# Optimization experiments

Measured on AMD Instinct MI355X. Metric: run time of the kernel, lower is better.

Reference implementation:

```python
import jax, jax.numpy as jnp
import numpy as np

EPS = 1e-8

def setup_inputs() -> dict:
    key = jax.random.key(0)
    ks = jax.random.split(key, 10)
    N, IN, Z, C, H = 8192, 512, 128, 64, 50
    x = jax.random.normal(ks[0], (N, IN), dtype=jnp.float32)
    c = jax.random.randint(ks[1], (N, 1), 0, C, dtype=jnp.int64)
    z = jax.random.normal(ks[2], (N, Z), dtype=jnp.float32)
    # f_x MLP params (Linear(IN,50) -> ReLU -> Linear(50,Z))
    W1 = jax.random.normal(ks[3], (IN, H), dtype=jnp.float32) / np.sqrt(IN)
    b1 = jax.random.normal(ks[4], (H,), dtype=jnp.float32) * 0.01
    W2 = jax.random.normal(ks[5], (H, Z), dtype=jnp.float32) / np.sqrt(H)
    b2 = jax.random.normal(ks[6], (Z,), dtype=jnp.float32) * 0.01
    # f_z Linear(Z,Z)
    Wz = jax.random.normal(ks[7], (Z, Z), dtype=jnp.float32) / np.sqrt(Z)
    bz = jax.random.normal(ks[8], (Z,), dtype=jnp.float32) * 0.01
    # per-category bilinear weights w_s [C,Z,Z] (torch.randn init)
    Ws = jax.random.normal(ks[9], (C, Z, Z), dtype=jnp.float32)
    return {"x": x, "c": c, "z": z, "W1": W1, "b1": b1, "W2": W2, "b2": b2, "Wz": Wz, "bz": bz, "Ws": Ws}

def reference(x, c, z, W1, b1, W2, b2, Wz, bz, Ws):
    cf = c.reshape(-1)                                    # [N]
    fx = jax.nn.relu(x @ W1 + b1) @ W2 + b2               # [N,Z]
    fz = z @ Wz + bz                                      # [N,Z]
    # per-sample bilinear: u[n] = fx[n] @ Ws[c[n]]
    u = jnp.einsum('nd,nde->ne', fx, Ws[cf])              # [N,Z]
    T = jax.nn.softplus(jnp.einsum('ne,ne->n', u, fz))    # [N]
    # neg_T[i] = mean over j with c[j]==c[i] of softplus(fx[i] @ Ws[c[i]] @ fz[j])
    S = jax.nn.softplus(u @ fz.T)                         # [N,N]
    mask = (cf[:, None] == cf[None, :]).astype(S.dtype)   # [N,N]
    neg_T = (S * mask).sum(axis=1) / mask.sum(axis=1)     # [N]
    return jnp.log(T + EPS) - jnp.log(neg_T + EPS)
```

## Files before the change

### kernel.cpp

```cpp
#include <hip/hip_runtime.h>
#include <math.h>

#define N_   8192
#define IN_  512
#define ZD   128
#define CC   64
#define HD   50
#define EPSF 1e-8f

typedef float vf4 __attribute__((ext_vector_type(4)));
typedef __attribute__((ext_vector_type(8))) short bfrag;

#define MFMA16(a, b, c) __builtin_amdgcn_mfma_f32_16x16x32_bf16((a), (b), (c), 0, 0, 0)

__device__ __forceinline__ float softplus_hot(float t) {
    return fmaxf(t, 0.f) + __logf(1.f + __expf(-fabsf(t)));
}
__device__ __forceinline__ float softplus_acc(float t) {
    return fmaxf(t, 0.f) + log1pf(expf(-fabsf(t)));
}
__device__ __forceinline__ unsigned short bf16_rn(float x) {
    unsigned int u = __float_as_uint(x);
    return (unsigned short)((u + 0x7fff + ((u >> 16) & 1)) >> 16);
}
__device__ __forceinline__ float bf16_f(unsigned short h) {
    return __uint_as_float(((unsigned int)h) << 16);
}
__device__ __forceinline__ void split8(const float* v, bfrag& hi, bfrag& lo) {
    #pragma unroll
    for (int e = 0; e < 8; ++e) {
        unsigned short h = bf16_rn(v[e]);
        ((short*)&hi)[e] = (short)h;
        ((short*)&lo)[e] = (short)bf16_rn(v[e] - bf16_f(h));
    }
}

__global__ __launch_bounds__(256) void k_pre(const int* __restrict__ c,
                                             const float* __restrict__ W1,
                                             const float* __restrict__ z,
                                             const float* __restrict__ Wz,
                                             const float* __restrict__ bz,
                                             const float* __restrict__ W2,
                                             const float* __restrict__ Ws,
                                             uint4* __restrict__ W1p,
                                             uint4* __restrict__ W2p,
                                             float* __restrict__ fz,
                                             unsigned short* __restrict__ fz_hi,
                                             unsigned short* __restrict__ Wst_hi,
                                             unsigned short* __restrict__ Wst_lo,
                                             int* __restrict__ counts,
                                             int* __restrict__ offsets,
                                             int* __restrict__ grouped) {
    __shared__ float smem[64 * 129];
    int tid = threadIdx.x;
    int b   = blockIdx.x;
    if (b < CC) {
        __shared__ int hist[CC];
        __shared__ int cursor;
        __shared__ int off_s;
        if (tid < CC) hist[tid] = 0;
        if (tid == 0) cursor = 0;
        __syncthreads();
        for (int i = tid; i < N_; i += 256) atomicAdd(&hist[c[i]], 1);
        __syncthreads();
        if (tid == 0) {
            int off = 0;
            for (int q = 0; q < b; ++q) off += hist[q];
            off_s = off;
            counts[b]  = hist[b];
            offsets[b] = off;
        }
        __syncthreads();
        int off = off_s;
        for (int i = tid; i < N_; i += 256) {
            if (c[i] == b) {
                int p = atomicAdd(&cursor, 1);
                grouped[off + p] = i;
            }
        }
    } else if (b < 80) {
        int unit = (b - 64) * 256 + tid;
        int lane = unit & 63, f = (unit >> 6) & 15, kc = unit >> 10;
        int nt = f >> 2, ks = f & 3;
        int n = nt * 16 + (lane & 15);
        int kbase = kc * 128 + ks * 32 + (lane >> 4) * 8;
        unsigned short hi8[8], lo8[8];
        #pragma unroll
        for (int j = 0; j < 8; ++j) {
            int k = kbase + j;
            float v = (n < HD) ? W1[k * HD + n] : 0.f;
            unsigned short h = bf16_rn(v);
            hi8[j] = h;
            lo8[j] = bf16_rn(v - bf16_f(h));
        }
        W1p[kc * 2048 + f * 64 + lane]        = *(uint4*)hi8;
        W1p[kc * 2048 + 1024 + f * 64 + lane] = *(uint4*)lo8;
    } else if (b < 84) {
        int unit = (b - 80) * 256 + tid;
        int lane = unit & 63, f = unit >> 6;
        int nt = f >> 1, ks = f & 1;
        int n = nt * 16 + (lane & 15);
        int kbase = ks * 32 + (lane >> 4) * 8;
        unsigned short hi8[8], lo8[8];
        #pragma unroll
        for (int j = 0; j < 8; ++j) {
            int k = kbase + j;
            float v = (k < HD) ? W2[k * ZD + n] : 0.f;
            unsigned short h = bf16_rn(v);
            hi8[j] = h;
            lo8[j] = bf16_rn(v - bf16_f(h));
        }
        W2p[f * 64 + lane]        = *(uint4*)hi8;
        W2p[1024 + f * 64 + lane] = *(uint4*)lo8;
    } else if (b < 212) {
        float* sz = smem;
        int row0 = (b - 84) * 64;
        vf4* s4 = (vf4*)sz;
        const vf4* z4 = (const vf4*)(z + (size_t)row0 * ZD);
        #pragma unroll
        for (int f = 0; f < 8; ++f) s4[tid + f * 256] = z4[tid + f * 256];
        __syncthreads();
        int cp = tid & 31, rgp = tid >> 5;
        const vf4* Wz4 = (const vf4*)Wz;
        vf4 bb = ((const vf4*)bz)[cp];
        vf4 acc[8];
        #pragma unroll
        for (int r = 0; r < 8; ++r) acc[r] = bb;
        #pragma unroll 1
        for (int d4 = 0; d4 < 32; ++d4) {
            vf4 w0 = Wz4[(4 * d4 + 0) * 32 + cp];
            vf4 w1 = Wz4[(4 * d4 + 1) * 32 + cp];
            vf4 w2 = Wz4[(4 * d4 + 2) * 32 + cp];
            vf4 w3 = Wz4[(4 * d4 + 3) * 32 + cp];
            #pragma unroll
            for (int r = 0; r < 8; ++r) {
                vf4 a = s4[(rgp * 8 + r) * 32 + d4];
                acc[r] += a[0] * w0;
                acc[r] += a[1] * w1;
                acc[r] += a[2] * w2;
                acc[r] += a[3] * w3;
            }
        }
        vf4* fz4 = (vf4*)fz;
        #pragma unroll
        for (int r = 0; r < 8; ++r) {
            int n = row0 + rgp * 8 + r;
            fz4[(size_t)n * 32 + cp] = acc[r];
            ushort4 h;
            h.x = bf16_rn(acc[r][0]); h.y = bf16_rn(acc[r][1]);
            h.z = bf16_rn(acc[r][2]); h.w = bf16_rn(acc[r][3]);
            *(ushort4*)(fz_hi + (size_t)n * ZD + cp * 4) = h;
        }
    } else {
        #pragma unroll 1
        for (int ci = 0; ci < 2; ++ci) {
            int cat = (b - 212) * 2 + ci;
            const float* Wc = Ws + (size_t)cat * ZD * ZD;
            unsigned short* Whi = Wst_hi + (size_t)cat * ZD * ZD;
            unsigned short* Wlo = Wst_lo + (size_t)cat * ZD * ZD;
            #pragma unroll 1
            for (int half = 0; half < 2; ++half) {
                __syncthreads();
                const vf4* src = (const vf4*)(Wc + (size_t)half * 64 * ZD);
                #pragma unroll
                for (int f = 0; f < 8; ++f) {
                    int idx = tid + f * 256;
                    int row = idx >> 5, q = idx & 31;
                    vf4 v = src[idx];
                    #pragma unroll
                    for (int e = 0; e < 4; ++e) smem[row * 129 + q * 4 + e] = v[e];
                }
                __syncthreads();
                #pragma unroll 1
                for (int f = 0; f < 32; ++f) {
                    int idx = tid + f * 256;
                    int e = idx >> 6, dd = idx & 63;
                    float v = smem[dd * 129 + e];
                    unsigned short h = bf16_rn(v);
                    Whi[(size_t)e * ZD + half * 64 + dd] = h;
                    Wlo[(size_t)e * ZD + half * 64 + dd] = bf16_rn(v - bf16_f(h));
                }
            }
        }
    }
}

__global__ __launch_bounds__(512) void k_hfx(const float* __restrict__ x,
                                             const uint4* __restrict__ W1p,
                                             const uint4* __restrict__ W2p,
                                             const float* __restrict__ b1,
                                             const float* __restrict__ b2,
                                             unsigned short* __restrict__ fx_hi,
                                             unsigned short* __restrict__ fx_lo) {
    __shared__ uint4 sW2[2048];
    __shared__ uint4 sW1[2048];
    __shared__ float sh[32 * 68];
    int tid = threadIdx.x;
    int lane = tid & 63, w = tid >> 6, m = lane & 15, quad = lane >> 4;
    int rg = w & 1, ch = w >> 1;
    int i0 = blockIdx.x * 32;

    #pragma unroll
    for (int f = 0; f < 4; ++f) sW2[tid + f * 512] = W2p[tid + f * 512];

    int row = i0 + rg * 16 + m;
    const float4* xr = (const float4*)(x + (size_t)row * IN_);

    vf4 accP = {0.f, 0.f, 0.f, 0.f};
    vf4 accQ = {0.f, 0.f, 0.f, 0.f};
    vf4 accR = {0.f, 0.f, 0.f, 0.f};

    #pragma unroll 1
    for (int kc = 0; kc < 4; ++kc) {
        __syncthreads();
        #pragma unroll
        for (int f = 0; f < 4; ++f)
            sW1[tid + f * 512] = W1p[kc * 2048 + tid + f * 512];
        __syncthreads();
        #pragma unroll 1
        for (int ks = 0; ks < 4; ++ks) {
            float4 xa = xr[kc * 32 + ks * 8 + quad * 2];
            float4 xb = xr[kc * 32 + ks * 8 + quad * 2 + 1];
            float xv[8] = {xa.x, xa.y, xa.z, xa.w, xb.x, xb.y, xb.z, xb.w};
            bfrag ah, al;
            split8(xv, ah, al);
            bfrag bh = *(const bfrag*)&sW1[(ch * 4 + ks) * 64 + lane];
            bfrag bl = *(const bfrag*)&sW1[1024 + (ch * 4 + ks) * 64 + lane];
            accP = MFMA16(ah, bh, accP);
            accQ = MFMA16(ah, bl, accQ);
            accR = MFMA16(al, bh, accR);
        }
    }
    {
        int col = ch * 16 + m;
        float bb = (col < HD) ? b1[col] : 0.f;
        vf4 acc = accP + accQ + accR;
        #pragma unroll
        for (int r = 0; r < 4; ++r)
            sh[(rg * 16 + quad * 4 + r) * 68 + col] = fmaxf(acc[r] + bb, 0.f);
    }
    __syncthreads();

    bfrag ah2[2], al2[2];
    #pragma unroll
    for (int ks = 0; ks < 2; ++ks) {
        const float4* shp = (const float4*)&sh[(rg * 16 + m) * 68 + ks * 32 + quad * 8];
        float4 ha = shp[0], hb = shp[1];
        float hv[8] = {ha.x, ha.y, ha.z, ha.w, hb.x, hb.y, hb.z, hb.w};
        split8(hv, ah2[ks], al2[ks]);
    }
    #pragma unroll
    for (int nt2 = 0; nt2 < 2; ++nt2) {
        int nt = ch * 2 + nt2;
        bfrag bh0 = *(const bfrag*)&sW2[(nt * 2 + 0) * 64 + lane];
        bfrag bl0 = *(const bfrag*)&sW2[1024 + (nt * 2 + 0) * 64 + lane];
        bfrag bh1 = *(const bfrag*)&sW2[(nt * 2 + 1) * 64 + lane];
        bfrag bl1 = *(const bfrag*)&sW2[1024 + (nt * 2 + 1) * 64 + lane];
        vf4 aA = {0.f, 0.f, 0.f, 0.f}, aB = {0.f, 0.f, 0.f, 0.f};
        aA = MFMA16(ah2[0], bh0, aA);
        aA = MFMA16(ah2[0], bl0, aA);
        aA = MFMA16(al2[0], bh0, aA);
        aB = MFMA16(ah2[1], bh1, aB);
        aB = MFMA16(ah2[1], bl1, aB);
        aB = MFMA16(al2[1], bh1, aB);
        vf4 a2 = aA + aB;
        int col = nt * 16 + m;
        float bb2 = b2[col];
        #pragma unroll
        for (int r = 0; r < 4; ++r) {
            size_t orow = (size_t)(i0 + rg * 16 + quad * 4 + r);
            float v = a2[r] + bb2;
            unsigned short hh = bf16_rn(v);
            fx_hi[orow * ZD + col] = hh;
            fx_lo[orow * ZD + col] = bf16_rn(v - bf16_f(hh));
        }
    }
}

#define TI 8
__global__ __launch_bounds__(512) void k_fused(const unsigned short* __restrict__ fx_hi,
                                               const unsigned short* __restrict__ fx_lo,
                                               const unsigned short* __restrict__ Wst_hi,
                                               const unsigned short* __restrict__ Wst_lo,
                                               const float* __restrict__ fz,
                                               const unsigned short* __restrict__ fz_hi,
                                               const int* __restrict__ grouped,
                                               const int* __restrict__ offsets,
                                               const int* __restrict__ counts,
                                               float* __restrict__ out) {
    __shared__ uint4 sWhi[128 * 17];
    __shared__ uint4 sWlo[128 * 17];
    __shared__ float sRed[2][4][16];
    int tid = threadIdx.x;
    int cat = blockIdx.x >> 3;
    int t   = blockIdx.x & (TI - 1);
    int off = offsets[cat], cnt = counts[cat];
    int i0 = t * 32;
    if (i0 >= cnt) return;
    int mI = min(32, cnt - i0);

    int lane = tid & 63, wave = tid >> 6;
    int m = lane & 15, quad = lane >> 4;
    int rg = wave & 1, eh = wave >> 1;

    const uint4* gh = (const uint4*)(Wst_hi + (size_t)cat * ZD * ZD);
    const uint4* gl = (const uint4*)(Wst_lo + (size_t)cat * ZD * ZD);
    #pragma unroll
    for (int f = 0; f < 4; ++f) {
        int idx = tid + f * 512;
        int e = idx >> 4, q = idx & 15;
        sWhi[e * 17 + q] = gh[idx];
        sWlo[e * 17 + q] = gl[idx];
    }

    int irow = rg * 16 + m;
    int n_gA = grouped[off + i0 + min(irow, mI - 1)];
    const unsigned short* fhp = fx_hi + (size_t)n_gA * ZD + quad * 8;
    const unsigned short* flp = fx_lo + (size_t)n_gA * ZD + quad * 8;
    bfrag a_hi[4], a_lo[4];
    #pragma unroll
    for (int kb = 0; kb < 4; ++kb) {
        a_hi[kb] = *(const bfrag*)(fhp + kb * 32);
        a_lo[kb] = *(const bfrag*)(flp + kb * 32);
    }
    __syncthreads();

    vf4 uacc[2];
    #pragma unroll 1
    for (int et2 = 0; et2 < 2; ++et2) {
        int et = eh * 2 + et2;
        vf4 aH = {0.f, 0.f, 0.f, 0.f};
        vf4 aM = {0.f, 0.f, 0.f, 0.f};
        vf4 aL = {0.f, 0.f, 0.f, 0.f};
        #pragma unroll
        for (int kb = 0; kb < 4; ++kb) {
            bfrag bh = *(const bfrag*)&sWhi[(et * 16 + m) * 17 + kb * 4 + quad];
            bfrag bl = *(const bfrag*)&sWlo[(et * 16 + m) * 17 + kb * 4 + quad];
            aH = MFMA16(a_hi[kb], bh, aH);
            aM = MFMA16(a_hi[kb], bl, aM);
            aL = MFMA16(a_lo[kb], bh, aL);
        }
        uacc[et2] = aH + aM + aL;
    }

    int nrow[4];
    #pragma unroll
    for (int r = 0; r < 4; ++r) {
        int ir = rg * 16 + quad * 4 + r;
        nrow[r] = (ir < mI) ? grouped[off + i0 + ir] : -1;
    }
    float fzv[2][4];
    #pragma unroll
    for (int et2 = 0; et2 < 2; ++et2) {
        #pragma unroll
        for (int r = 0; r < 4; ++r) {
            fzv[et2][r] = 0.f;
            if (nrow[r] >= 0)
                fzv[et2][r] = fz[(size_t)nrow[r] * ZD + (eh * 2 + et2) * 16 + m];
        }
    }
    float p[4] = {0.f, 0.f, 0.f, 0.f};
    #pragma unroll
    for (int et2 = 0; et2 < 2; ++et2) {
        #pragma unroll
        for (int r = 0; r < 4; ++r) p[r] += uacc[et2][r] * fzv[et2][r];
    }
    #pragma unroll
    for (int r = 0; r < 4; ++r) {
        float v = p[r];
        #pragma unroll
        for (int s = 8; s >= 1; s >>= 1) v += __shfl_xor(v, s, 64);
        p[r] = v;
    }
    if (m == 0) {
        #pragma unroll
        for (int r = 0; r < 4; ++r) sRed[rg][eh][quad * 4 + r] = p[r];
    }
    __syncthreads();

    unsigned short* su = (unsigned short*)sWhi;
    #pragma unroll
    for (int et2 = 0; et2 < 2; ++et2) {
        int col = (eh * 2 + et2) * 16 + m;
        #pragma unroll
        for (int r = 0; r < 4; ++r)
            su[(rg * 16 + quad * 4 + r) * 136 + col] = bf16_rn(uacc[et2][r]);
    }
    float logT_r[4] = {0.f, 0.f, 0.f, 0.f};
    if (eh == 0) {
        #pragma unroll
        for (int r = 0; r < 4; ++r) {
            float pt = sRed[rg][0][quad * 4 + r] + sRed[rg][1][quad * 4 + r]
                     + sRed[rg][2][quad * 4 + r] + sRed[rg][3][quad * 4 + r];
            logT_r[r] = logf(softplus_acc(pt) + EPSF);
        }
    }
    __syncthreads();

    bfrag na[4];
    #pragma unroll
    for (int kb = 0; kb < 4; ++kb)
        na[kb] = *(const bfrag*)&su[(rg * 16 + m) * 136 + kb * 32 + quad * 8];

    uint4* sB = (uint4*)sWlo;
    float negsum[4] = {0.f, 0.f, 0.f, 0.f};

    #pragma unroll 1
    for (int jb = 0; jb < cnt; jb += 64) {
        int mJ = min(64, cnt - jb);
        __syncthreads();
        #pragma unroll
        for (int f = 0; f < 2; ++f) {
            int idx = tid + f * 512;
            int jr = idx >> 4, q = idx & 15;
            uint4 v = {0u, 0u, 0u, 0u};
            if (jr < mJ) {
                int j_g = grouped[off + jb + jr];
                v = *(const uint4*)(fz_hi + (size_t)j_g * ZD + q * 8);
            }
            sB[jr * 17 + q] = v;
        }
        __syncthreads();
        {
            int jt = eh;
            bfrag b0 = *(const bfrag*)&sB[(jt * 16 + m) * 17 + 0 + quad];
            bfrag b1 = *(const bfrag*)&sB[(jt * 16 + m) * 17 + 4 + quad];
            bfrag b2 = *(const bfrag*)&sB[(jt * 16 + m) * 17 + 8 + quad];
            bfrag b3 = *(const bfrag*)&sB[(jt * 16 + m) * 17 + 12 + quad];
            vf4 aA = {0.f, 0.f, 0.f, 0.f}, aB = {0.f, 0.f, 0.f, 0.f};
            aA = MFMA16(na[0], b0, aA);
            aA = MFMA16(na[1], b1, aA);
            aB = MFMA16(na[2], b2, aB);
            aB = MFMA16(na[3], b3, aB);
            vf4 acc = aA + aB;
            bool jok = (jt * 16 + m) < mJ;
            #pragma unroll
            for (int r = 0; r < 4; ++r)
                if (jok) negsum[r] += softplus_hot(acc[r]);
        }
    }

    #pragma unroll
    for (int r = 0; r < 4; ++r) {
        float v = negsum[r];
        #pragma unroll
        for (int s = 8; s >= 1; s >>= 1) v += __shfl_xor(v, s, 64);
        negsum[r] = v;
    }
    if (m == 0) {
        #pragma unroll
        for (int r = 0; r < 4; ++r) sRed[rg][eh][quad * 4 + r] = negsum[r];
    }
    __syncthreads();
    if (eh == 0 && m == 0) {
        #pragma unroll
        for (int r = 0; r < 4; ++r) {
            if (nrow[r] >= 0) {
                float tot = sRed[rg][0][quad * 4 + r] + sRed[rg][1][quad * 4 + r]
                          + sRed[rg][2][quad * 4 + r] + sRed[rg][3][quad * 4 + r];
                out[nrow[r]] = logT_r[r] - logf(tot / (float)cnt + EPSF);
            }
        }
    }
}

extern "C" void kernel_launch(void* const* d_in, const int* in_sizes, int n_in,
                              void* d_out, int out_size, void* d_ws, size_t ws_size,
                              hipStream_t stream) {
    const float* x  = (const float*)d_in[0];
    const int*   c  = (const int*)  d_in[1];
    const float* z  = (const float*)d_in[2];
    const float* W1 = (const float*)d_in[3];
    const float* b1 = (const float*)d_in[4];
    const float* W2 = (const float*)d_in[5];
    const float* b2 = (const float*)d_in[6];
    const float* Wz = (const float*)d_in[7];
    const float* bz = (const float*)d_in[8];
    const float* Ws = (const float*)d_in[9];
    float* out = (float*)d_out;

    uint4* W1p = (uint4*)d_ws;
    uint4* W2p = W1p + 8192;
    float* fz  = (float*)(W2p + 2048);
    unsigned short* fx_hi  = (unsigned short*)(fz + (size_t)N_ * ZD);
    unsigned short* fx_lo  = fx_hi + (size_t)N_ * ZD;
    unsigned short* fz_hi  = fx_lo + (size_t)N_ * ZD;
    unsigned short* Wst_hi = fz_hi + (size_t)N_ * ZD;
    unsigned short* Wst_lo = Wst_hi + (size_t)CC * ZD * ZD;
    int* counts  = (int*)(Wst_lo + (size_t)CC * ZD * ZD);
    int* offsets = counts + CC;
    int* grouped = offsets + CC;

    k_pre   <<<244, 256, 0, stream>>>(c, W1, z, Wz, bz, W2, Ws, W1p, W2p, fz,
                                      fz_hi, Wst_hi, Wst_lo, counts, offsets,
                                      grouped);
    k_hfx   <<<N_ / 32, 512, 0, stream>>>(x, W1p, W2p, b1, b2, fx_hi, fx_lo);
    k_fused <<<CC * TI, 512, 0, stream>>>(fx_hi, fx_lo, Wst_hi, Wst_lo, fz,
                                          fz_hi, grouped, offsets, counts, out);
}
```

Before: 131.2 us.

## Merge three kernels into one cooperative persistent kernel with grid syncs

```diff
diff --git a/kernel.cpp b/kernel.cpp
--- a/kernel.cpp
+++ b/kernel.cpp
@@ -1,5 +1,8 @@
 #include <hip/hip_runtime.h>
+#include <hip/hip_cooperative_groups.h>
 #include <math.h>
+
+namespace cg = cooperative_groups;
 
 #define N_   8192
 #define IN_  512
@@ -35,51 +38,65 @@
     }
 }
 
-__global__ __launch_bounds__(256) void k_pre(const int* __restrict__ c,
-                                             const float* __restrict__ W1,
-                                             const float* __restrict__ z,
-                                             const float* __restrict__ Wz,
-                                             const float* __restrict__ bz,
-                                             const float* __restrict__ W2,
-                                             const float* __restrict__ Ws,
-                                             uint4* __restrict__ W1p,
-                                             uint4* __restrict__ W2p,
-                                             float* __restrict__ fz,
-                                             unsigned short* __restrict__ fz_hi,
-                                             unsigned short* __restrict__ Wst_hi,
-                                             unsigned short* __restrict__ Wst_lo,
-                                             int* __restrict__ counts,
-                                             int* __restrict__ offsets,
-                                             int* __restrict__ grouped) {
-    __shared__ float smem[64 * 129];
+#define OFF_A 0
+#define OFF_B 34816
+#define OFF_C 69632
+#define OFF_D 78336
+#define OFF_E 95744
+
+__global__ __launch_bounds__(512) void k_mega(const int* __restrict__ c,
+                                              const float* __restrict__ x,
+                                              const float* __restrict__ z,
+                                              const float* __restrict__ W1,
+                                              const float* __restrict__ b1,
+                                              const float* __restrict__ W2,
+                                              const float* __restrict__ b2,
+                                              const float* __restrict__ Wz,
+                                              const float* __restrict__ bz,
+                                              const float* __restrict__ Ws,
+                                              uint4* __restrict__ W1p,
+                                              uint4* __restrict__ W2p,
+                                              float* __restrict__ fz,
+                                              unsigned short* __restrict__ fx_hi,
+                                              unsigned short* __restrict__ fx_lo,
+                                              unsigned short* __restrict__ fz_hi,
+                                              unsigned short* __restrict__ Wst_hi,
+                                              unsigned short* __restrict__ Wst_lo,
+                                              int* __restrict__ counts,
+                                              int* __restrict__ offsets,
+                                              int* __restrict__ grouped,
+                                              float* __restrict__ out) {
+    __shared__ __align__(16) unsigned char SM[96256];
+    cg::grid_group grid = cg::this_grid();
     int tid = threadIdx.x;
     int b   = blockIdx.x;
+
     if (b < CC) {
-        __shared__ int hist[CC];
-        __shared__ int cursor;
-        __shared__ int off_s;
+        int* hist   = (int*)(SM + OFF_B);
+        int* cursor = (int*)(SM + OFF_B + 256);
+        int* off_s  = (int*)(SM + OFF_B + 260);
         if (tid < CC) hist[tid] = 0;
-        if (tid == 0) cursor = 0;
+        if (tid == 0) *cursor = 0;
         __syncthreads();
-        for (int i = tid; i < N_; i += 256) atomicAdd(&hist[c[i]], 1);
+        for (int i = tid; i < N_; i += 512) atomicAdd(&hist[c[i]], 1);
         __syncthreads();
         if (tid == 0) {
             int off = 0;
             for (int q = 0; q < b; ++q) off += hist[q];
-            off_s = off;
+            *off_s = off;
             counts[b]  = hist[b];
             offsets[b] = off;
         }
         __syncthreads();
-        int off = off_s;
-        for (int i = tid; i < N_; i += 256) {
+        int off = *off_s;
+        for (int i = tid; i < N_; i += 512) {
             if (c[i] == b) {
-                int p = atomicAdd(&cursor, 1);
+                int p = atomicAdd(cursor, 1);
                 grouped[off + p] = i;
             }
         }
-    } else if (b < 80) {
-        int unit = (b - 64) * 256 + tid;
+    } else if (b < 72) {
+        int unit = (b - 64) * 512 + tid;
         int lane = unit & 63, f = (unit >> 6) & 15, kc = unit >> 10;
         int nt = f >> 2, ks = f & 3;
         int n = nt * 16 + (lane & 15);
@@ -95,8 +112,8 @@
         }
         W1p[kc * 2048 + f * 64 + lane]        = *(uint4*)hi8;
         W1p[kc * 2048 + 1024 + f * 64 + lane] = *(uint4*)lo8;
-    } else if (b < 84) {
-        int unit = (b - 80) * 256 + tid;
+    } else if (b < 74) {
+        int unit = (b - 72) * 512 + tid;
         int lane = unit & 63, f = unit >> 6;
         int nt = f >> 1, ks = f & 1;
         int n = nt * 16 + (lane & 15);
@@ -112,20 +129,20 @@
         }
         W2p[f * 64 + lane]        = *(uint4*)hi8;
         W2p[1024 + f * 64 + lane] = *(uint4*)lo8;
-    } else if (b < 212) {
-        float* sz = smem;
-        int row0 = (b - 84) * 64;
+    } else if (b < 202) {
+        float* sz = (float*)(SM + OFF_A);
+        int row0 = (b - 74) * 64;
         vf4* s4 = (vf4*)sz;
         const vf4* z4 = (const vf4*)(z + (size_t)row0 * ZD);
         #pragma unroll
-        for (int f = 0; f < 8; ++f) s4[tid + f * 256] = z4[tid + f * 256];
+        for (int f = 0; f < 4; ++f) s4[tid + f * 512] = z4[tid + f * 512];
         __syncthreads();
         int cp = tid & 31, rgp = tid >> 5;
         const vf4* Wz4 = (const vf4*)Wz;
         vf4 bb = ((const vf4*)bz)[cp];
-        vf4 acc[8];
-        #pragma unroll
-        for (int r = 0; r < 8; ++r) acc[r] = bb;
+        vf4 acc[4];
+        #pragma unroll
+        for (int r = 0; r < 4; ++r) acc[r] = bb;
         #pragma unroll 1
         for (int d4 = 0; d4 < 32; ++d4) {
             vf4 w0 = Wz4[(4 * d4 + 0) * 32 + cp];
@@ -133,8 +150,8 @@
             vf4 w2 = Wz4[(4 * d4 + 2) * 32 + cp];
             vf4 w3 = Wz4[(4 * d4 + 3) * 32 + cp];
             #pragma unroll
-            for (int r = 0; r < 8; ++r) {
-                vf4 a = s4[(rgp * 8 + r) * 32 + d4];
+            for (int r = 0; r < 4; ++r) {
+                vf4 a = s4[(rgp * 4 + r) * 32 + d4];
                 acc[r] += a[0] * w0;
                 acc[r] += a[1] * w1;
                 acc[r] += a[2] * w2;
@@ -143,18 +160,19 @@
         }
         vf4* fz4 = (vf4*)fz;
         #pragma unroll
-        for (int r = 0; r < 8; ++r) {
-            int n = row0 + rgp * 8 + r;
+        for (int r = 0; r < 4; ++r) {
+            int n = row0 + rgp * 4 + r;
             fz4[(size_t)n * 32 + cp] = acc[r];
             ushort4 h;
             h.x = bf16_rn(acc[r][0]); h.y = bf16_rn(acc[r][1]);
             h.z = bf16_rn(acc[r][2]); h.w = bf16_rn(acc[r][3]);
             *(ushort4*)(fz_hi + (size_t)n * ZD + cp * 4) = h;
         }
-    } else {
+    } else if (b < 234) {
+        float* smem = (float*)(SM + OFF_A);
         #pragma unroll 1
         for (int ci = 0; ci < 2; ++ci) {
-            int cat = (b - 212) * 2 + ci;
+            int cat = (b - 202) * 2 + ci;
             const float* Wc = Ws + (size_t)cat * ZD * ZD;
             unsigned short* Whi = Wst_hi + (size_t)cat * ZD * ZD;
             unsigned short* Wlo = Wst_lo + (size_t)cat * ZD * ZD;
@@ -163,8 +181,8 @@
                 __syncthreads();
                 const vf4* src = (const vf4*)(Wc + (size_t)half * 64 * ZD);
                 #pragma unroll
-                for (int f = 0; f < 8; ++f) {
-                    int idx = tid + f * 256;
+                for (int f = 0; f < 4; ++f) {
+                    int idx = tid + f * 512;
                     int row = idx >> 5, q = idx & 31;
                     vf4 v = src[idx];
                     #pragma unroll
@@ -172,8 +190,8 @@
                 }
                 __syncthreads();
                 #pragma unroll 1
-                for (int f = 0; f < 32; ++f) {
-                    int idx = tid + f * 256;
+                for (int f = 0; f < 16; ++f) {
+                    int idx = tid + f * 512;
                     int e = idx >> 6, dd = idx & 63;
                     float v = smem[dd * 129 + e];
                     unsigned short h = bf16_rn(v);
@@ -183,282 +201,282 @@
             }
         }
     }
-}
-
-__global__ __launch_bounds__(512) void k_hfx(const float* __restrict__ x,
-                                             const uint4* __restrict__ W1p,
-                                             const uint4* __restrict__ W2p,
-                                             const float* __restrict__ b1,
-                                             const float* __restrict__ b2,
-                                             unsigned short* __restrict__ fx_hi,
-                                             unsigned short* __restrict__ fx_lo) {
-    __shared__ uint4 sW2[2048];
-    __shared__ uint4 sW1[2048];
-    __shared__ float sh[32 * 68];
-    int tid = threadIdx.x;
-    int lane = tid & 63, w = tid >> 6, m = lane & 15, quad = lane >> 4;
-    int rg = w & 1, ch = w >> 1;
-    int i0 = blockIdx.x * 32;
-
-    #pragma unroll
-    for (int f = 0; f < 4; ++f) sW2[tid + f * 512] = W2p[tid + f * 512];
-
-    int row = i0 + rg * 16 + m;
-    const float4* xr = (const float4*)(x + (size_t)row * IN_);
-
-    vf4 accP = {0.f, 0.f, 0.f, 0.f};
-    vf4 accQ = {0.f, 0.f, 0.f, 0.f};
-    vf4 accR = {0.f, 0.f, 0.f, 0.f};
-
-    #pragma unroll 1
-    for (int kc = 0; kc < 4; ++kc) {
-        __syncthreads();
-        #pragma unroll
-        for (int f = 0; f < 4; ++f)
-            sW1[tid + f * 512] = W1p[kc * 2048 + tid + f * 512];
-        __syncthreads();
+
+    __threadfence();
+    grid.sync();
+
+    {
+        uint4* sW2 = (uint4*)(SM + OFF_A);
+        uint4* sW1 = (uint4*)(SM + OFF_B);
+        float* sh  = (float*)(SM + OFF_C);
+        int lane = tid & 63, w = tid >> 6, m = lane & 15, quad = lane >> 4;
+        int rg = w & 1, ch = w >> 1;
+        int i0 = b * 32;
+
+        #pragma unroll
+        for (int f = 0; f < 4; ++f) sW2[tid + f * 512] = W2p[tid + f * 512];
+
+        int row = i0 + rg * 16 + m;
+        const float4* xr = (const float4*)(x + (size_t)row * IN_);
+
+        vf4 accP = {0.f, 0.f, 0.f, 0.f};
+        vf4 accQ = {0.f, 0.f, 0.f, 0.f};
+        vf4 accR = {0.f, 0.f, 0.f, 0.f};
+
         #pragma unroll 1
-        for (int ks = 0; ks < 4; ++ks) {
-            float4 xa = xr[kc * 32 + ks * 8 + quad * 2];
-            float4 xb = xr[kc * 32 + ks * 8 + quad * 2 + 1];
-            float xv[8] = {xa.x, xa.y, xa.z, xa.w, xb.x, xb.y, xb.z, xb.w};
-            bfrag ah, al;
-            split8(xv, ah, al);
-            bfrag bh = *(const bfrag*)&sW1[(ch * 4 + ks) * 64 + lane];
-            bfrag bl = *(const bfrag*)&sW1[1024 + (ch * 4 + ks) * 64 + lane];
-            accP = MFMA16(ah, bh, accP);
-            accQ = MFMA16(ah, bl, accQ);
-            accR = MFMA16(al, bh, accR);
-        }
-    }
-    {
-        int col = ch * 16 + m;
-        float bb = (col < HD) ? b1[col] : 0.f;
-        vf4 acc = accP + accQ + accR;
-        #pragma unroll
-        for (int r = 0; r < 4; ++r)
-            sh[(rg * 16 + quad * 4 + r) * 68 + col] = fmaxf(acc[r] + bb, 0.f);
-    }
-    __syncthreads();
-
-    bfrag ah2[2], al2[2];
-    #pragma unroll
-    for (int ks = 0; ks < 2; ++ks) {
-        const float4* shp = (const float4*)&sh[(rg * 16 + m) * 68 + ks * 32 + quad * 8];
-        float4 ha = shp[0], hb = shp[1];
-        float hv[8] = {ha.x, ha.y, ha.z, ha.w, hb.x, hb.y, hb.z, hb.w};
-        split8(hv, ah2[ks], al2[ks]);
-    }
-    #pragma unroll
-    for (int nt2 = 0; nt2 < 2; ++nt2) {
-        int nt = ch * 2 + nt2;
-        bfrag bh0 = *(const bfrag*)&sW2[(nt * 2 + 0) * 64 + lane];
-        bfrag bl0 = *(const bfrag*)&sW2[1024 + (nt * 2 + 0) * 64 + lane];
-        bfrag bh1 = *(const bfrag*)&sW2[(nt * 2 + 1) * 64 + lane];
-        bfrag bl1 = *(const bfrag*)&sW2[1024 + (nt * 2 + 1) * 64 + lane];
-        vf4 aA = {0.f, 0.f, 0.f, 0.f}, aB = {0.f, 0.f, 0.f, 0.f};
-        aA = MFMA16(ah2[0], bh0, aA);
-        aA = MFMA16(ah2[0], bl0, aA);
-        aA = MFMA16(al2[0], bh0, aA);
-        aB = MFMA16(ah2[1], bh1, aB);
-        aB = MFMA16(ah2[1], bl1, aB);
-        aB = MFMA16(al2[1], bh1, aB);
-        vf4 a2 = aA + aB;
-        int col = nt * 16 + m;
-        float bb2 = b2[col];
-        #pragma unroll
-        for (int r = 0; r < 4; ++r) {
-            size_t orow = (size_t)(i0 + rg * 16 + quad * 4 + r);
-            float v = a2[r] + bb2;
-            unsigned short hh = bf16_rn(v);
-            fx_hi[orow * ZD + col] = hh;
-            fx_lo[orow * ZD + col] = bf16_rn(v - bf16_f(hh));
-        }
-    }
-}
-
-#define TI 8
-__global__ __launch_bounds__(512) void k_fused(const unsigned short* __restrict__ fx_hi,
-                                               const unsigned short* __restrict__ fx_lo,
-                                               const unsigned short* __restrict__ Wst_hi,
-                                               const unsigned short* __restrict__ Wst_lo,
-                                               const float* __restrict__ fz,
-                                               const unsigned short* __restrict__ fz_hi,
-                                               const int* __restrict__ grouped,
-                                               const int* __restrict__ offsets,
-                                               const int* __restrict__ counts,
-                                               float* __restrict__ out) {
-    __shared__ uint4 sWhi[128 * 17];
-    __shared__ uint4 sWlo[128 * 17];
-    __shared__ float sRed[2][4][16];
-    int tid = threadIdx.x;
-    int cat = blockIdx.x >> 3;
-    int t   = blockIdx.x & (TI - 1);
-    int off = offsets[cat], cnt = counts[cat];
-    int i0 = t * 32;
-    if (i0 >= cnt) return;
-    int mI = min(32, cnt - i0);
-
-    int lane = tid & 63, wave = tid >> 6;
-    int m = lane & 15, quad = lane >> 4;
-    int rg = wave & 1, eh = wave >> 1;
-
-    const uint4* gh = (const uint4*)(Wst_hi + (size_t)cat * ZD * ZD);
-    const uint4* gl = (const uint4*)(Wst_lo + (size_t)cat * ZD * ZD);
-    #pragma unroll
-    for (int f = 0; f < 4; ++f) {
-        int idx = tid + f * 512;
-        int e = idx >> 4, q = idx & 15;
-        sWhi[e * 17 + q] = gh[idx];
-        sWlo[e * 17 + q] = gl[idx];
-    }
-
-    int irow = rg * 16 + m;
-    int n_gA = grouped[off + i0 + min(irow, mI - 1)];
-    const unsigned short* fhp = fx_hi + (size_t)n_gA * ZD + quad * 8;
-    const unsigned short* flp = fx_lo + (size_t)n_gA * ZD + quad * 8;
-    bfrag a_hi[4], a_lo[4];
-    #pragma unroll
-    for (int kb = 0; kb < 4; ++kb) {
-        a_hi[kb] = *(const bfrag*)(fhp + kb * 32);
-        a_lo[kb] = *(const bfrag*)(flp + kb * 32);
-    }
-    __syncthreads();
-
-    vf4 uacc[2];
-    #pragma unroll 1
-    for (int et2 = 0; et2 < 2; ++et2) {
-        int et = eh * 2 + et2;
-        vf4 aH = {0.f, 0.f, 0.f, 0.f};
-        vf4 aM = {0.f, 0.f, 0.f, 0.f};
-        vf4 aL = {0.f, 0.f, 0.f, 0.f};
-        #pragma unroll
-        for (int kb = 0; kb < 4; ++kb) {
-            bfrag bh = *(const bfrag*)&sWhi[(et * 16 + m) * 17 + kb * 4 + quad];
-            bfrag bl = *(const bfrag*)&sWlo[(et * 16 + m) * 17 + kb * 4 + quad];
-            aH = MFMA16(a_hi[kb], bh, aH);
-            aM = MFMA16(a_hi[kb], bl, aM);
-            aL = MFMA16(a_lo[kb], bh, aL);
-        }
-        uacc[et2] = aH + aM + aL;
-    }
-
-    int nrow[4];
-    #pragma unroll
-    for (int r = 0; r < 4; ++r) {
-        int ir = rg * 16 + quad * 4 + r;
-        nrow[r] = (ir < mI) ? grouped[off + i0 + ir] : -1;
-    }
-    float fzv[2][4];
-    #pragma unroll
-    for (int et2 = 0; et2 < 2; ++et2) {
-        #pragma unroll
-        for (int r = 0; r < 4; ++r) {
-            fzv[et2][r] = 0.f;
-            if (nrow[r] >= 0)
-                fzv[et2][r] = fz[(size_t)nrow[r] * ZD + (eh * 2 + et2) * 16 + m];
-        }
-    }
-    float p[4] = {0.f, 0.f, 0.f, 0.f};
-    #pragma unroll
-    for (int et2 = 0; et2 < 2; ++et2) {
-        #pragma unroll
-        for (int r = 0; r < 4; ++r) p[r] += uacc[et2][r] * fzv[et2][r];
-    }
-    #pragma unroll
-    for (int r = 0; r < 4; ++r) {
-        float v = p[r];
-        #pragma unroll
-        for (int s = 8; s >= 1; s >>= 1) v += __shfl_xor(v, s, 64);
-        p[r] = v;
-    }
-    if (m == 0) {
-        #pragma unroll
-        for (int r = 0; r < 4; ++r) sRed[rg][eh][quad * 4 + r] = p[r];
-    }
-    __syncthreads();
-
-    unsigned short* su = (unsigned short*)sWhi;
-    #pragma unroll
-    for (int et2 = 0; et2 < 2; ++et2) {
-        int col = (eh * 2 + et2) * 16 + m;
-        #pragma unroll
-        for (int r = 0; r < 4; ++r)
-            su[(rg * 16 + quad * 4 + r) * 136 + col] = bf16_rn(uacc[et2][r]);
-    }
-    float logT_r[4] = {0.f, 0.f, 0.f, 0.f};
-    if (eh == 0) {
-        #pragma unroll
-        for (int r = 0; r < 4; ++r) {
-            float pt = sRed[rg][0][quad * 4 + r] + sRed[rg][1][quad * 4 + r]
-                     + sRed[rg][2][quad * 4 + r] + sRed[rg][3][quad * 4 + r];
-            logT_r[r] = logf(softplus_acc(pt) + EPSF);
-        }
-    }
-    __syncthreads();
-
-    bfrag na[4];
-    #pragma unroll
-    for (int kb = 0; kb < 4; ++kb)
-        na[kb] = *(const bfrag*)&su[(rg * 16 + m) * 136 + kb * 32 + quad * 8];
-
-    uint4* sB = (uint4*)sWlo;
-    float negsum[4] = {0.f, 0.f, 0.f, 0.f};
-
-    #pragma unroll 1
-    for (int jb = 0; jb < cnt; jb += 64) {
-        int mJ = min(64, cnt - jb);
-        __syncthreads();
-        #pragma unroll
-        for (int f = 0; f < 2; ++f) {
-            int idx = tid + f * 512;
-            int jr = idx >> 4, q = idx & 15;
-            uint4 v = {0u, 0u, 0u, 0u};
-            if (jr < mJ) {
-                int j_g = grouped[off + jb + jr];
-                v = *(const uint4*)(fz_hi + (size_t)j_g * ZD + q * 8);
-            }
-            sB[jr * 17 + q] = v;
-        }
-        __syncthreads();
+        for (int kc = 0; kc < 4; ++kc) {
+            __syncthreads();
+            #pragma unroll
+            for (int f = 0; f < 4; ++f)
+                sW1[tid + f * 512] = W1p[kc * 2048 + tid + f * 512];
+            __syncthreads();
+            #pragma unroll 1
+            for (int ks = 0; ks < 4; ++ks) {
+                float4 xa = xr[kc * 32 + ks * 8 + quad * 2];
+                float4 xb = xr[kc * 32 + ks * 8 + quad * 2 + 1];
+                float xv[8] = {xa.x, xa.y, xa.z, xa.w, xb.x, xb.y, xb.z, xb.w};
+                bfrag ah, al;
+                split8(xv, ah, al);
+                bfrag bh = *(const bfrag*)&sW1[(ch * 4 + ks) * 64 + lane];
+                bfrag bl = *(const bfrag*)&sW1[1024 + (ch * 4 + ks) * 64 + lane];
+                accP = MFMA16(ah, bh, accP);
+                accQ = MFMA16(ah, bl, accQ);
+                accR = MFMA16(al, bh, accR);
+            }
+        }
         {
-            int jt = eh;
-            bfrag b0 = *(const bfrag*)&sB[(jt * 16 + m) * 17 + 0 + quad];
-            bfrag b1 = *(const bfrag*)&sB[(jt * 16 + m) * 17 + 4 + quad];
-            bfrag b2 = *(const bfrag*)&sB[(jt * 16 + m) * 17 + 8 + quad];
-            bfrag b3 = *(const bfrag*)&sB[(jt * 16 + m) * 17 + 12 + quad];
-            vf4 aA = {0.f, 0.f, 0.f, 0.f}, aB = {0.f, 0.f, 0.f, 0.f};
-            aA = MFMA16(na[0], b0, aA);
-            aA = MFMA16(na[1], b1, aA);
-            aB = MFMA16(na[2], b2, aB);
-            aB = MFMA16(na[3], b3, aB);
-            vf4 acc = aA + aB;
-            bool jok = (jt * 16 + m) < mJ;
+            int col = ch * 16 + m;
+            float bb = (col < HD) ? b1[col] : 0.f;
+            vf4 acc = accP + accQ + accR;
             #pragma unroll
             for (int r = 0; r < 4; ++r)
-                if (jok) negsum[r] += softplus_hot(acc[r]);
+                sh[(rg * 16 + quad * 4 + r) * 68 + col] = fmaxf(acc[r] + bb, 0.f);
+        }
+        __syncthreads();
+
+        bfrag ah2[2], al2[2];
+        #pragma unroll
+        for (int ks = 0; ks < 2; ++ks) {
+            const float4* shp = (const float4*)&sh[(rg * 16 + m) * 68 + ks * 32 + quad * 8];
+            float4 ha = shp[0], hb = shp[1];
+            float hv[8] = {ha.x, ha.y, ha.z, ha.w, hb.x, hb.y, hb.z, hb.w};
+            split8(hv, ah2[ks], al2[ks]);
+        }
+        #pragma unroll
+        for (int nt2 = 0; nt2 < 2; ++nt2) {
+            int nt = ch * 2 + nt2;
+            bfrag bh0 = *(const bfrag*)&sW2[(nt * 2 + 0) * 64 + lane];
+            bfrag bl0 = *(const bfrag*)&sW2[1024 + (nt * 2 + 0) * 64 + lane];
+            bfrag bh1 = *(const bfrag*)&sW2[(nt * 2 + 1) * 64 + lane];
+            bfrag bl1 = *(const bfrag*)&sW2[1024 + (nt * 2 + 1) * 64 + lane];
+            vf4 aA = {0.f, 0.f, 0.f, 0.f}, aB = {0.f, 0.f, 0.f, 0.f};
+            aA = MFMA16(ah2[0], bh0, aA);
+            aA = MFMA16(ah2[0], bl0, aA);
+            aA = MFMA16(al2[0], bh0, aA);
+            aB = MFMA16(ah2[1], bh1, aB);
+            aB = MFMA16(ah2[1], bl1, aB);
+            aB = MFMA16(al2[1], bh1, aB);
+            vf4 a2 = aA + aB;
+            int col = nt * 16 + m;
+            float bb2 = b2[col];
+            #pragma unroll
+            for (int r = 0; r < 4; ++r) {
+                size_t orow = (size_t)(i0 + rg * 16 + quad * 4 + r);
+                float v = a2[r] + bb2;
+                unsigned short hh = bf16_rn(v);
+                fx_hi[orow * ZD + col] = hh;
+                fx_lo[orow * ZD + col] = bf16_rn(v - bf16_f(hh));
+            }
         }
     }
 
-    #pragma unroll
-    for (int r = 0; r < 4; ++r) {
-        float v = negsum[r];
-        #pragma unroll
-        for (int s = 8; s >= 1; s >>= 1) v += __shfl_xor(v, s, 64);
-        negsum[r] = v;
-    }
-    if (m == 0) {
-        #pragma unroll
-        for (int r = 0; r < 4; ++r) sRed[rg][eh][quad * 4 + r] = negsum[r];
-    }
-    __syncthreads();
-    if (eh == 0 && m == 0) {
-        #pragma unroll
-        for (int r = 0; r < 4; ++r) {
-            if (nrow[r] >= 0) {
-                float tot = sRed[rg][0][quad * 4 + r] + sRed[rg][1][quad * 4 + r]
-                          + sRed[rg][2][quad * 4 + r] + sRed[rg][3][quad * 4 + r];
-                out[nrow[r]] = logT_r[r] - logf(tot / (float)cnt + EPSF);
+    __threadfence();
+    grid.sync();
+
+    {
+        int cat = b >> 2;
+        int tq  = b & 3;
+        int off = offsets[cat], cnt = counts[cat];
+        if (tq * 32 < cnt) {
+            uint4* sWhi = (uint4*)(SM + OFF_A);
+            uint4* sWlo = (uint4*)(SM + OFF_B);
+            unsigned short* su = (unsigned short*)(SM + OFF_C);
+            uint4* sB = (uint4*)(SM + OFF_D);
+            float* sRedF = (float*)(SM + OFF_E);
+
+            int lane = tid & 63, wave = tid >> 6;
+            int m = lane & 15, quad = lane >> 4;
+            int rg = wave & 1, eh = wave >> 1;
+
+            const uint4* gh = (const uint4*)(Wst_hi + (size_t)cat * ZD * ZD);
+            const uint4* gl = (const uint4*)(Wst_lo + (size_t)cat * ZD * ZD);
+            #pragma unroll
+            for (int f = 0; f < 4; ++f) {
+                int idx = tid + f * 512;
+                int e = idx >> 4, q = idx & 15;
+                sWhi[e * 17 + q] = gh[idx];
+                sWlo[e * 17 + q] = gl[idx];
+            }
+            __syncthreads();
+
+            #pragma unroll 1
+            for (int tt = 0; tt < 2; ++tt) {
+                int i0 = (tq + tt * 4) * 32;
+                if (i0 >= cnt) break;
+                int mI = min(32, cnt - i0);
+                __syncthreads();
+
+                int irow = rg * 16 + m;
+                int n_gA = grouped[off + i0 + min(irow, mI - 1)];
+                const unsigned short* fhp = fx_hi + (size_t)n_gA * ZD + quad * 8;
+                const unsigned short* flp = fx_lo + (size_t)n_gA * ZD + quad * 8;
+                bfrag a_hi[4], a_lo[4];
+                #pragma unroll
+                for (int kb = 0; kb < 4; ++kb) {
+                    a_hi[kb] = *(const bfrag*)(fhp + kb * 32);
+                    a_lo[kb] = *(const bfrag*)(flp + kb * 32);
+                }
+
+                vf4 uacc[2];
+                #pragma unroll 1
+                for (int et2 = 0; et2 < 2; ++et2) {
+                    int et = eh * 2 + et2;
+                    vf4 aH = {0.f, 0.f, 0.f, 0.f};
+                    vf4 aM = {0.f, 0.f, 0.f, 0.f};
+                    vf4 aL = {0.f, 0.f, 0.f, 0.f};
+                    #pragma unroll
+                    for (int kb = 0; kb < 4; ++kb) {
+                        bfrag bh = *(const bfrag*)&sWhi[(et * 16 + m) * 17 + kb * 4 + quad];
+                        bfrag bl = *(const bfrag*)&sWlo[(et * 16 + m) * 17 + kb * 4 + quad];
+                        aH = MFMA16(a_hi[kb], bh, aH);
+                        aM = MFMA16(a_hi[kb], bl, aM);
+                        aL = MFMA16(a_lo[kb], bh, aL);
+                    }
+                    uacc[et2] = aH + aM + aL;
+                }
+
+                int nrow[4];
+                #pragma unroll
+                for (int r = 0; r < 4; ++r) {
+                    int ir = rg * 16 + quad * 4 + r;
+                    nrow[r] = (ir < mI) ? grouped[off + i0 + ir] : -1;
+                }
+                float fzv[2][4];
+                #pragma unroll
+                for (int et2 = 0; et2 < 2; ++et2) {
+                    #pragma unroll
+                    for (int r = 0; r < 4; ++r) {
+                        fzv[et2][r] = 0.f;
+                        if (nrow[r] >= 0)
+                            fzv[et2][r] = fz[(size_t)nrow[r] * ZD + (eh * 2 + et2) * 16 + m];
+                    }
+                }
+                float p[4] = {0.f, 0.f, 0.f, 0.f};
+                #pragma unroll
+                for (int et2 = 0; et2 < 2; ++et2) {
+                    #pragma unroll
+                    for (int r = 0; r < 4; ++r) p[r] += uacc[et2][r] * fzv[et2][r];
+                }
+                #pragma unroll
+                for (int r = 0; r < 4; ++r) {
+                    float v = p[r];
+                    #pragma unroll
+                    for (int s = 8; s >= 1; s >>= 1) v += __shfl_xor(v, s, 64);
+                    p[r] = v;
+                }
+                if (m == 0) {
+                    #pragma unroll
+                    for (int r = 0; r < 4; ++r)
+                        sRedF[(rg * 4 + eh) * 16 + quad * 4 + r] = p[r];
+                }
+                __syncthreads();
+
+                #pragma unroll
+                for (int et2 = 0; et2 < 2; ++et2) {
+                    int col = (eh * 2 + et2) * 16 + m;
+                    #pragma unroll
+                    for (int r = 0; r < 4; ++r)
+                        su[(rg * 16 + quad * 4 + r) * 136 + col] = bf16_rn(uacc[et2][r]);
+                }
+                float logT_r[4] = {0.f, 0.f, 0.f, 0.f};
+                if (eh == 0) {
+                    #pragma unroll
+                    for (int r = 0; r < 4; ++r) {
+                        float pt = sRedF[(rg * 4 + 0) * 16 + quad * 4 + r]
+                                 + sRedF[(rg * 4 + 1) * 16 + quad * 4 + r]
+                                 + sRedF[(rg * 4 + 2) * 16 + quad * 4 + r]
+                                 + sRedF[(rg * 4 + 3) * 16 + quad * 4 + r];
+                        logT_r[r] = logf(softplus_acc(pt) + EPSF);
+                    }
+                }
+                __syncthreads();
+
+                bfrag na[4];
+                #pragma unroll
+                for (int kb = 0; kb < 4; ++kb)
+                    na[kb] = *(const bfrag*)&su[(rg * 16 + m) * 136 + kb * 32 + quad * 8];
+
+                float negsum[4] = {0.f, 0.f, 0.f, 0.f};
+                #pragma unroll 1
+                for (int jb = 0; jb < cnt; jb += 64) {
+                    int mJ = min(64, cnt - jb);
+                    __syncthreads();
+                    #pragma unroll
+                    for (int f = 0; f < 2; ++f) {
+                        int idx = tid + f * 512;
+                        int jr = idx >> 4, q = idx & 15;
+                        uint4 v = {0u, 0u, 0u, 0u};
+                        if (jr < mJ) {
+                            int j_g = grouped[off + jb + jr];
+                            v = *(const uint4*)(fz_hi + (size_t)j_g * ZD + q * 8);
+                        }
+                        sB[jr * 17 + q] = v;
+                    }
+                    __syncthreads();
+                    {
+                        int jt = eh;
+                        bfrag b0 = *(const bfrag*)&sB[(jt * 16 + m) * 17 + 0 + quad];
+                        bfrag b1 = *(const bfrag*)&sB[(jt * 16 + m) * 17 + 4 + quad];
+                        bfrag b2 = *(const bfrag*)&sB[(jt * 16 + m) * 17 + 8 + quad];
+                        bfrag b3 = *(const bfrag*)&sB[(jt * 16 + m) * 17 + 12 + quad];
+                        vf4 aA = {0.f, 0.f, 0.f, 0.f}, aB = {0.f, 0.f, 0.f, 0.f};
+                        aA = MFMA16(na[0], b0, aA);
+                        aA = MFMA16(na[1], b1, aA);
+                        aB = MFMA16(na[2], b2, aB);
+                        aB = MFMA16(na[3], b3, aB);
+                        vf4 acc = aA + aB;
+                        bool jok = (jt * 16 + m) < mJ;
+                        #pragma unroll
+                        for (int r = 0; r < 4; ++r)
+                            if (jok) negsum[r] += softplus_hot(acc[r]);
+                    }
+                }
+
+                #pragma unroll
+                for (int r = 0; r < 4; ++r) {
+                    float v = negsum[r];
+                    #pragma unroll
+                    for (int s = 8; s >= 1; s >>= 1) v += __shfl_xor(v, s, 64);
+                    negsum[r] = v;
+                }
+                if (m == 0) {
+                    #pragma unroll
+                    for (int r = 0; r < 4; ++r)
+                        sRedF[(rg * 4 + eh) * 16 + quad * 4 + r] = negsum[r];
+                }
+                __syncthreads();
+                if (eh == 0 && m == 0) {
+                    #pragma unroll
+                    for (int r = 0; r < 4; ++r) {
+                        if (nrow[r] >= 0) {
+                            float tot = sRedF[(rg * 4 + 0) * 16 + quad * 4 + r]
+                                      + sRedF[(rg * 4 + 1) * 16 + quad * 4 + r]
+                                      + sRedF[(rg * 4 + 2) * 16 + quad * 4 + r]
+                                      + sRedF[(rg * 4 + 3) * 16 + quad * 4 + r];
+                            out[nrow[r]] = logT_r[r] - logf(tot / (float)cnt + EPSF);
+                        }
+                    }
+                }
             }
         }
     }
@@ -467,8 +485,8 @@
 extern "C" void kernel_launch(void* const* d_in, const int* in_sizes, int n_in,
                               void* d_out, int out_size, void* d_ws, size_t ws_size,
                               hipStream_t stream) {
+    const int*   c  = (const int*)  d_in[1];
     const float* x  = (const float*)d_in[0];
-    const int*   c  = (const int*)  d_in[1];
     const float* z  = (const float*)d_in[2];
     const float* W1 = (const float*)d_in[3];
     const float* b1 = (const float*)d_in[4];
@@ -491,10 +509,13 @@
     int* offsets = counts + CC;
     int* grouped = offsets + CC;
 
-    k_pre   <<<244, 256, 0, stream>>>(c, W1, z, Wz, bz, W2, Ws, W1p, W2p, fz,
-                                      fz_hi, Wst_hi, Wst_lo, counts, offsets,
-                                      grouped);
-    k_hfx   <<<N_ / 32, 512, 0, stream>>>(x, W1p, W2p, b1, b2, fx_hi, fx_lo);
-    k_fused <<<CC * TI, 512, 0, stream>>>(fx_hi, fx_lo, Wst_hi, Wst_lo, fz,
-                                          fz_hi, grouped, offsets, counts, out);
-}
+    void* kargs[] = {
+        (void*)&c,  (void*)&x,  (void*)&z,  (void*)&W1, (void*)&b1,
+        (void*)&W2, (void*)&b2, (void*)&Wz, (void*)&bz, (void*)&Ws,
+        (void*)&W1p, (void*)&W2p, (void*)&fz, (void*)&fx_hi, (void*)&fx_lo,
+        (void*)&fz_hi, (void*)&Wst_hi, (void*)&Wst_lo,
+        (void*)&counts, (void*)&offsets, (void*)&grouped, (void*)&out
+    };
+    hipLaunchCooperativeKernel((void*)k_mega, dim3(256), dim3(512), kargs, 0,
+                               stream);
+}
```

After: 318.1 us. +142.4%, slower.

## Fuse f_x MLP kernel into per-category bilinear kernel via shared memory

Applied to the files above, without the earlier changes.

```diff
diff --git a/kernel.cpp b/kernel.cpp
--- a/kernel.cpp
+++ b/kernel.cpp
@@ -185,26 +185,48 @@
     }
 }
 
-__global__ __launch_bounds__(512) void k_hfx(const float* __restrict__ x,
+#define TI 8
+__global__ __launch_bounds__(512) void k_all(const float* __restrict__ x,
                                              const uint4* __restrict__ W1p,
                                              const uint4* __restrict__ W2p,
                                              const float* __restrict__ b1,
                                              const float* __restrict__ b2,
-                                             unsigned short* __restrict__ fx_hi,
-                                             unsigned short* __restrict__ fx_lo) {
-    __shared__ uint4 sW2[2048];
-    __shared__ uint4 sW1[2048];
-    __shared__ float sh[32 * 68];
+                                             const unsigned short* __restrict__ Wst_hi,
+                                             const unsigned short* __restrict__ Wst_lo,
+                                             const float* __restrict__ fz,
+                                             const unsigned short* __restrict__ fz_hi,
+                                             const int* __restrict__ grouped,
+                                             const int* __restrict__ offsets,
+                                             const int* __restrict__ counts,
+                                             float* __restrict__ out) {
+    __shared__ __align__(16) unsigned char SM[78848];
+    uint4* A4    = (uint4*)(SM);
+    uint4* B4    = (uint4*)(SM + 34816);
+    float* shC   = (float*)(SM + 69632);
+    float* sRedF = (float*)(SM + 78336);
+
     int tid = threadIdx.x;
-    int lane = tid & 63, w = tid >> 6, m = lane & 15, quad = lane >> 4;
-    int rg = w & 1, ch = w >> 1;
-    int i0 = blockIdx.x * 32;
+    int cat = blockIdx.x >> 3;
+    int t   = blockIdx.x & (TI - 1);
+    int off = offsets[cat], cnt = counts[cat];
+    int i0 = t * 32;
+    if (i0 >= cnt) return;
+    int mI = min(32, cnt - i0);
+
+    int lane = tid & 63, wave = tid >> 6;
+    int m = lane & 15, quad = lane >> 4;
+    int rg = wave & 1, ch = wave >> 1;
+
+    uint4* sW2 = A4;
+    uint4* sW1 = B4;
+    float* sh  = shC;
 
     #pragma unroll
     for (int f = 0; f < 4; ++f) sW2[tid + f * 512] = W2p[tid + f * 512];
 
-    int row = i0 + rg * 16 + m;
-    const float4* xr = (const float4*)(x + (size_t)row * IN_);
+    int irowA = rg * 16 + m;
+    int n_gA = grouped[off + i0 + min(irowA, mI - 1)];
+    const float4* xr = (const float4*)(x + (size_t)n_gA * IN_);
 
     vf4 accP = {0.f, 0.f, 0.f, 0.f};
     vf4 accQ = {0.f, 0.f, 0.f, 0.f};
@@ -249,6 +271,10 @@
         float hv[8] = {ha.x, ha.y, ha.z, ha.w, hb.x, hb.y, hb.z, hb.w};
         split8(hv, ah2[ks], al2[ks]);
     }
+    __syncthreads();
+
+    unsigned short* fxhiT = (unsigned short*)shC;
+    unsigned short* fxloT = (unsigned short*)B4;
     #pragma unroll
     for (int nt2 = 0; nt2 < 2; ++nt2) {
         int nt = ch * 2 + nt2;
@@ -264,45 +290,30 @@
         aB = MFMA16(ah2[1], bl1, aB);
         aB = MFMA16(al2[1], bh1, aB);
         vf4 a2 = aA + aB;
-        int col = nt * 16 + m;
-        float bb2 = b2[col];
+        int colB = nt * 16 + m;
+        float bb2 = b2[colB];
         #pragma unroll
         for (int r = 0; r < 4; ++r) {
-            size_t orow = (size_t)(i0 + rg * 16 + quad * 4 + r);
+            int row = rg * 16 + quad * 4 + r;
             float v = a2[r] + bb2;
             unsigned short hh = bf16_rn(v);
-            fx_hi[orow * ZD + col] = hh;
-            fx_lo[orow * ZD + col] = bf16_rn(v - bf16_f(hh));
-        }
-    }
-}
-
-#define TI 8
-__global__ __launch_bounds__(512) void k_fused(const unsigned short* __restrict__ fx_hi,
-                                               const unsigned short* __restrict__ fx_lo,
-                                               const unsigned short* __restrict__ Wst_hi,
-                                               const unsigned short* __restrict__ Wst_lo,
-                                               const float* __restrict__ fz,
-                                               const unsigned short* __restrict__ fz_hi,
-                                               const int* __restrict__ grouped,
-                                               const int* __restrict__ offsets,
-                                               const int* __restrict__ counts,
-                                               float* __restrict__ out) {
-    __shared__ uint4 sWhi[128 * 17];
-    __shared__ uint4 sWlo[128 * 17];
-    __shared__ float sRed[2][4][16];
-    int tid = threadIdx.x;
-    int cat = blockIdx.x >> 3;
-    int t   = blockIdx.x & (TI - 1);
-    int off = offsets[cat], cnt = counts[cat];
-    int i0 = t * 32;
-    if (i0 >= cnt) return;
-    int mI = min(32, cnt - i0);
-
-    int lane = tid & 63, wave = tid >> 6;
-    int m = lane & 15, quad = lane >> 4;
-    int rg = wave & 1, eh = wave >> 1;
-
+            fxhiT[row * 136 + colB] = hh;
+            fxloT[row * 136 + colB] = bf16_rn(v - bf16_f(hh));
+        }
+    }
+    __syncthreads();
+
+    int eh = ch;
+    bfrag a_hi[4], a_lo[4];
+    #pragma unroll
+    for (int kb = 0; kb < 4; ++kb) {
+        a_hi[kb] = *(const bfrag*)&fxhiT[(rg * 16 + m) * 136 + kb * 32 + quad * 8];
+        a_lo[kb] = *(const bfrag*)&fxloT[(rg * 16 + m) * 136 + kb * 32 + quad * 8];
+    }
+    __syncthreads();
+
+    uint4* sWhi = A4;
+    uint4* sWlo = B4;
     const uint4* gh = (const uint4*)(Wst_hi + (size_t)cat * ZD * ZD);
     const uint4* gl = (const uint4*)(Wst_lo + (size_t)cat * ZD * ZD);
     #pragma unroll
@@ -311,17 +322,6 @@
         int e = idx >> 4, q = idx & 15;
         sWhi[e * 17 + q] = gh[idx];
         sWlo[e * 17 + q] = gl[idx];
-    }
-
-    int irow = rg * 16 + m;
-    int n_gA = grouped[off + i0 + min(irow, mI - 1)];
-    const unsigned short* fhp = fx_hi + (size_t)n_gA * ZD + quad * 8;
-    const unsigned short* flp = fx_lo + (size_t)n_gA * ZD + quad * 8;
-    bfrag a_hi[4], a_lo[4];
-    #pragma unroll
-    for (int kb = 0; kb < 4; ++kb) {
-        a_hi[kb] = *(const bfrag*)(fhp + kb * 32);
-        a_lo[kb] = *(const bfrag*)(flp + kb * 32);
     }
     __syncthreads();
 
@@ -374,11 +374,12 @@
     }
     if (m == 0) {
         #pragma unroll
-        for (int r = 0; r < 4; ++r) sRed[rg][eh][quad * 4 + r] = p[r];
-    }
-    __syncthreads();
-
-    unsigned short* su = (unsigned short*)sWhi;
+        for (int r = 0; r < 4; ++r)
+            sRedF[(rg * 4 + eh) * 16 + quad * 4 + r] = p[r];
+    }
+    __syncthreads();
+
+    unsigned short* su = (unsigned short*)A4;
     #pragma unroll
     for (int et2 = 0; et2 < 2; ++et2) {
         int col = (eh * 2 + et2) * 16 + m;
@@ -390,8 +391,10 @@
     if (eh == 0) {
         #pragma unroll
         for (int r = 0; r < 4; ++r) {
-            float pt = sRed[rg][0][quad * 4 + r] + sRed[rg][1][quad * 4 + r]
-                     + sRed[rg][2][quad * 4 + r] + sRed[rg][3][quad * 4 + r];
+            float pt = sRedF[(rg * 4 + 0) * 16 + quad * 4 + r]
+                     + sRedF[(rg * 4 + 1) * 16 + quad * 4 + r]
+                     + sRedF[(rg * 4 + 2) * 16 + quad * 4 + r]
+                     + sRedF[(rg * 4 + 3) * 16 + quad * 4 + r];
             logT_r[r] = logf(softplus_acc(pt) + EPSF);
         }
     }
@@ -402,7 +405,7 @@
     for (int kb = 0; kb < 4; ++kb)
         na[kb] = *(const bfrag*)&su[(rg * 16 + m) * 136 + kb * 32 + quad * 8];
 
-    uint4* sB = (uint4*)sWlo;
+    uint4* sB = B4;
     float negsum[4] = {0.f, 0.f, 0.f, 0.f};
 
     #pragma unroll 1
@@ -449,15 +452,18 @@
     }
     if (m == 0) {
         #pragma unroll
-        for (int r = 0; r < 4; ++r) sRed[rg][eh][quad * 4 + r] = negsum[r];
+        for (int r = 0; r < 4; ++r)
+            sRedF[(rg * 4 + eh) * 16 + quad * 4 + r] = negsum[r];
     }
     __syncthreads();
     if (eh == 0 && m == 0) {
         #pragma unroll
         for (int r = 0; r < 4; ++r) {
             if (nrow[r] >= 0) {
-                float tot = sRed[rg][0][quad * 4 + r] + sRed[rg][1][quad * 4 + r]
-                          + sRed[rg][2][quad * 4 + r] + sRed[rg][3][quad * 4 + r];
+                float tot = sRedF[(rg * 4 + 0) * 16 + quad * 4 + r]
+                          + sRedF[(rg * 4 + 1) * 16 + quad * 4 + r]
+                          + sRedF[(rg * 4 + 2) * 16 + quad * 4 + r]
+                          + sRedF[(rg * 4 + 3) * 16 + quad * 4 + r];
                 out[nrow[r]] = logT_r[r] - logf(tot / (float)cnt + EPSF);
             }
         }
@@ -482,19 +488,17 @@
     uint4* W1p = (uint4*)d_ws;
     uint4* W2p = W1p + 8192;
     float* fz  = (float*)(W2p + 2048);
-    unsigned short* fx_hi  = (unsigned short*)(fz + (size_t)N_ * ZD);
-    unsigned short* fx_lo  = fx_hi + (size_t)N_ * ZD;
-    unsigned short* fz_hi  = fx_lo + (size_t)N_ * ZD;
+    unsigned short* fz_hi  = (unsigned short*)(fz + (size_t)N_ * ZD);
     unsigned short* Wst_hi = fz_hi + (size_t)N_ * ZD;
     unsigned short* Wst_lo = Wst_hi + (size_t)CC * ZD * ZD;
     int* counts  = (int*)(Wst_lo + (size_t)CC * ZD * ZD);
     int* offsets = counts + CC;
     int* grouped = offsets + CC;
 
-    k_pre   <<<244, 256, 0, stream>>>(c, W1, z, Wz, bz, W2, Ws, W1p, W2p, fz,
-                                      fz_hi, Wst_hi, Wst_lo, counts, offsets,
-                                      grouped);
-    k_hfx   <<<N_ / 32, 512, 0, stream>>>(x, W1p, W2p, b1, b2, fx_hi, fx_lo);
-    k_fused <<<CC * TI, 512, 0, stream>>>(fx_hi, fx_lo, Wst_hi, Wst_lo, fz,
-                                          fz_hi, grouped, offsets, counts, out);
-}
+    k_pre <<<244, 256, 0, stream>>>(c, W1, z, Wz, bz, W2, Ws, W1p, W2p, fz,
+                                    fz_hi, Wst_hi, Wst_lo, counts, offsets,
+                                    grouped);
+    k_all <<<CC * TI, 512, 0, stream>>>(x, W1p, W2p, b1, b2, Wst_hi, Wst_lo,
+                                        fz, fz_hi, grouped, offsets, counts,
+                                        out);
+}
```

Result: no change. 132.2 us (+0.7%).
